# Performance work log

Hardware: AMD Instinct MI355X
Metric: run time of the kernel (lower is better)

Reference implementation:

```python
import jax, jax.numpy as jnp
import numpy as np
from jax.scipy.linalg import solve_triangular, cho_solve

K_SPARSE = 5
COMMIT = 0.25
EPS = 1e-10


def batch_omp(X, D, K):
    """Batched Orthogonal Matching Pursuit.
    X: [C, M] signals (columns). D: [C, N] L2-normalized dictionary.
    Returns support [M, K] (int32) and coefficients [M, K] in selection order.
    """
    G = D.T @ D                    # [N, N] Gram matrix
    h_bar = (D.T @ X).T            # [M, N] correlations
    M, N = h_bar.shape
    h = h_bar
    mask = jnp.ones((M, N), dtype=bool)
    gamma = jnp.zeros_like(h_bar)
    L = jnp.ones((M, 1, 1), dtype=X.dtype)
    rows = jnp.arange(M)
    I = None
    for k in range(1, K + 1):  # K is small and static -> unrolled
        idx = jnp.argmax(jnp.abs(h) * mask, axis=1)          # [M]
        mask = mask.at[rows, idx].set(False)
        if k > 1:
            G_col = G[I, idx[:, None]]                        # [M, k-1]
            w = solve_triangular(L, G_col[..., None], lower=True)[..., 0]  # [M, k-1]
            corner = jnp.sqrt(jnp.clip(1.0 - jnp.sum(w * w, axis=1), 1e-12))  # [M]
            top = jnp.concatenate([L, jnp.zeros((M, k - 1, 1), X.dtype)], axis=2)
            bot = jnp.concatenate([w[:, None, :], corner[:, None, None]], axis=2)
            L = jnp.concatenate([top, bot], axis=1)           # [M, k, k]
            I = jnp.concatenate([I, idx[:, None]], axis=1)
        else:
            I = idx[:, None]
        h_sel = h_bar[rows[:, None], I]                       # [M, k]
        gamma_sel = cho_solve((L, True), h_sel[..., None])[..., 0]  # [M, k]
        gamma = gamma.at[rows[:, None], I].set(gamma_sel)
        # beta = gamma_sel @ G[I]  -> residual update over all atoms
        beta = jnp.einsum('mk,mkn->mn', gamma_sel, G[I])      # [M, N]
        h = h_bar - beta
    coeffs = gamma[rows[:, None], I]                          # [M, K]
    return I, coeffs


def setup_inputs() -> dict:
    key = jax.random.key(0)
    k1, k2 = jax.random.split(key)
    z_e = jax.random.normal(k1, (8, 64, 64, 64), dtype=jnp.float32)        # [B, C, H, W]
    dictionary = jax.random.normal(k2, (64, 512), dtype=jnp.float32)       # [C, N]
    return {"z_e": z_e, "dictionary": dictionary}


def reference(z_e, dictionary):
    B, C, H, W = z_e.shape
    # [B,C,H,W] -> [C, B*H*W] column signals
    signals = z_e.transpose(0, 2, 3, 1).reshape(-1, C).T
    # L2-normalize dictionary columns (F.normalize with dim=0)
    norms = jnp.linalg.norm(dictionary, axis=0, keepdims=True)
    Dn = dictionary / jnp.maximum(norms, EPS)
    # OMP runs under no_grad in the original
    support, coeffs = batch_omp(jax.lax.stop_gradient(signals),
                                jax.lax.stop_gradient(Dn), K_SPARSE)
    # reconstruct: sum_k coeff_k * atom_k (gradient flows through Dn)
    atoms = Dn.T[support]                                     # [M, K, C]
    recon = jnp.einsum('mkc,mk->mc', atoms, coeffs)           # [M, C]
    z_dl = recon.reshape(B, H, W, C).transpose(0, 3, 1, 2)    # [B, C, H, W]
    dl_latent_loss = jnp.mean((z_dl - jax.lax.stop_gradient(z_e)) ** 2)
    e_latent_loss = jnp.mean((jax.lax.stop_gradient(z_dl) - z_e) ** 2)
    loss = dl_latent_loss + COMMIT * e_latent_loss
    z_dl_ste = z_e + jax.lax.stop_gradient(z_dl - z_e)        # straight-through
    return (z_dl_ste, loss,
            support.reshape(B, H, W, K_SPARSE),
            coeffs.reshape(B, H, W, K_SPARSE))
```

## Files before the change

### kernel.cpp

```cpp
#include <hip/hip_runtime.h>

#define NC 64
#define NA 512
#define KS 5

#define WS_DN   0
#define WS_DNT  32768
#define WS_G    65536
#define WS_ACCF 327680

#define OUT_LOSS 2097152
#define OUT_SUP  2097153
#define OUT_COF  2260993

__global__ void norm_kernel(const float* __restrict__ D, float* __restrict__ Dn,
                            float* __restrict__ DnT) {
  int n = blockIdx.x * 64 + threadIdx.x;
  float s = 0.f;
  for (int c = 0; c < NC; ++c) {
    float v = D[c * NA + n];
    s += v * v;
  }
  float den = fmaxf(sqrtf(s), 1e-10f);
  for (int c = 0; c < NC; ++c) {
    float v = D[c * NA + n] / den;
    Dn[c * NA + n]  = v;
    DnT[n * NC + c] = v;
  }
}

__global__ void gram_kernel(const float* __restrict__ Dn,
                            float* __restrict__ G, double* __restrict__ accum) {
  __shared__ float col[NC];
  int i = blockIdx.x, t = threadIdx.x;
  if (t < NC) col[t] = Dn[t * NA + i];
  if (i == 0 && t == 0) *accum = 0.0;
  __syncthreads();
  float s = 0.f;
#pragma unroll
  for (int c = 0; c < NC; ++c) s += col[c] * Dn[c * NA + t];
  G[(size_t)i * NA + t] = s;
}

template<int KK>
__device__ __forceinline__ void omp_stepH(
    const int hl, const float* __restrict__ G,
    const float* __restrict__ parkS,
    float (&h16)[16], unsigned &msk, int (&I)[KS],
    float (&Lo)[10], float (&rd)[KS], float (&gam)[KS]) {
  float bv = -1.f; int bn = 0;
#pragma unroll
  for (int s = 0; s < 16; ++s) {
    int a = ((s >> 2) << 7) + 4 * hl + (s & 3);
    float v = ((msk >> s) & 1u) ? fabsf(h16[s]) : 0.f;
    if (v > bv) { bv = v; bn = a; }
  }
#pragma unroll
  for (int off = 1; off < 32; off <<= 1) {
    float ov = __shfl_xor(bv, off);
    int   on = __shfl_xor(bn, off);
    if (ov > bv || (ov == bv && on < bn)) { bv = ov; bn = on; }
  }
  const int idx = bn;
  if (((idx & 127) >> 2) == hl)
    msk &= ~(1u << (((idx >> 7) << 2) | (idx & 3)));
  I[KK] = idx;

  if constexpr (KK == 0) {
    rd[0] = 1.f;
  } else {
    float Gc[KK], w_[KK];
#pragma unroll
    for (int j = 0; j < KK; ++j) Gc[j] = G[(size_t)I[j] * NA + idx];
#pragma unroll
    for (int i = 0; i < KK; ++i) {
      float ssum = Gc[i];
#pragma unroll
      for (int j = 0; j < i; ++j) ssum -= Lo[i*(i-1)/2 + j] * w_[j];
      w_[i] = ssum * rd[i];
    }
    float ww = 0.f;
#pragma unroll
    for (int i = 0; i < KK; ++i) ww += w_[i] * w_[i];
    float corner = sqrtf(fmaxf(1.f - ww, 1e-12f));
#pragma unroll
    for (int j = 0; j < KK; ++j) Lo[KK*(KK-1)/2 + j] = w_[j];
    rd[KK] = 1.f / corner;
  }

#pragma unroll
  for (int i = 0; i <= KK; ++i) {
    float b_ = parkS[I[i]];
#pragma unroll
    for (int j = 0; j < i; ++j) b_ -= Lo[i*(i-1)/2 + j] * gam[j];
    gam[i] = b_ * rd[i];
  }
#pragma unroll
  for (int i = KK; i >= 0; --i) {
    float g_ = gam[i];
#pragma unroll
    for (int j = i + 1; j <= KK; ++j) g_ -= Lo[j*(j-1)/2 + i] * gam[j];
    gam[i] = g_ * rd[i];
  }

  if constexpr (KK < 4) {
    const float4* pk4 = (const float4*)parkS;
#pragma unroll
    for (int i = 0; i < 4; ++i) {
      float4 hv = pk4[(i << 5) + hl];
      h16[i*4+0] = hv.x; h16[i*4+1] = hv.y; h16[i*4+2] = hv.z; h16[i*4+3] = hv.w;
    }
#pragma unroll
    for (int j = 0; j <= KK; ++j) {
      const float4* g4 = (const float4*)(G + (size_t)I[j] * NA);
      const float gj = gam[j];
#pragma unroll
      for (int i = 0; i < 4; ++i) {
        float4 g = g4[(i << 5) + hl];
        h16[i*4+0] -= gj * g.x; h16[i*4+1] -= gj * g.y;
        h16[i*4+2] -= gj * g.z; h16[i*4+3] -= gj * g.w;
      }
    }
  }
}

__global__ __launch_bounds__(256, 4) void omp_kernel(
    const float* __restrict__ z, const float* __restrict__ Dn,
    const float* __restrict__ DnT, const float* __restrict__ G,
    float* __restrict__ out, double* __restrict__ accum) {
  __shared__ __align__(16) float park[8 * NA];
  __shared__ float xsz[8 * NC];
  __shared__ double wsq[8];
  const int t = threadIdx.x, lane = t & 63, wv = t >> 6;
  const int hl = lane & 31;
  const int m0 = blockIdx.x * 8;
  const int bh = m0 >> 6, b = bh >> 6, h = bh & 63, w0 = m0 & 63;
  const size_t zbase = (size_t)b * 262144 + (size_t)h * 64 + w0;

  for (int j = t; j < 8 * NC; j += 256) {
    int c = j >> 3, s = j & 7;
    xsz[s * NC + c] = z[zbase + (size_t)c * 4096 + s];
  }
  __syncthreads();
  const int sig = wv * 2 + (lane >> 5);
  const float2 xf2 = *(const float2*)&xsz[sig * NC + 2 * hl];

  {
    float acc[8][2];
#pragma unroll
    for (int s = 0; s < 8; ++s) { acc[s][0] = 0.f; acc[s][1] = 0.f; }

    const float2* Dn2 = (const float2*)Dn + (wv << 6) + lane;
    const float4* zp4 = (const float4*)(z + zbase);
#pragma unroll 8
    for (int c = 0; c < 64; ++c) {
      float2 dv = Dn2[c << 8];
      float4 xa = zp4[(c << 10)];
      float4 xb = zp4[(c << 10) + 1];
      acc[0][0] += xa.x * dv.x; acc[0][1] += xa.x * dv.y;
      acc[1][0] += xa.y * dv.x; acc[1][1] += xa.y * dv.y;
      acc[2][0] += xa.z * dv.x; acc[2][1] += xa.z * dv.y;
      acc[3][0] += xa.w * dv.x; acc[3][1] += xa.w * dv.y;
      acc[4][0] += xb.x * dv.x; acc[4][1] += xb.x * dv.y;
      acc[5][0] += xb.y * dv.x; acc[5][1] += xb.y * dv.y;
      acc[6][0] += xb.z * dv.x; acc[6][1] += xb.z * dv.y;
      acc[7][0] += xb.w * dv.x; acc[7][1] += xb.w * dv.y;
    }
    float2* park2 = (float2*)park;
#pragma unroll
    for (int s = 0; s < 8; ++s)
      park2[(s << 8) + (wv << 6) + lane] = make_float2(acc[s][0], acc[s][1]);
  }
  __syncthreads();

  const float* parkS = park + (size_t)sig * NA;
  float h16[16];
  {
    const float4* pk4 = (const float4*)parkS;
#pragma unroll
    for (int i = 0; i < 4; ++i) {
      float4 hv = pk4[(i << 5) + hl];
      h16[i*4+0] = hv.x; h16[i*4+1] = hv.y; h16[i*4+2] = hv.z; h16[i*4+3] = hv.w;
    }
  }
  unsigned msk = 0xFFFFu;
  int I[KS];
  float Lo[10], rd[KS], gam[KS];

  omp_stepH<0>(hl, G, parkS, h16, msk, I, Lo, rd, gam);
  omp_stepH<1>(hl, G, parkS, h16, msk, I, Lo, rd, gam);
  omp_stepH<2>(hl, G, parkS, h16, msk, I, Lo, rd, gam);
  omp_stepH<3>(hl, G, parkS, h16, msk, I, Lo, rd, gam);
  omp_stepH<4>(hl, G, parkS, h16, msk, I, Lo, rd, gam);

  float rrA = 0.f, rrB = 0.f;
#pragma unroll
  for (int j = 0; j < KS; ++j) {
    const float2 dvv = ((const float2*)(DnT + (size_t)I[j] * NC))[hl];
    rrA += gam[j] * dvv.x;
    rrB += gam[j] * dvv.y;
  }
  const float dA = rrA - xf2.x, dB = rrB - xf2.y;
  xsz[(2 * hl) * 8 + sig]     = xf2.x + dA;
  xsz[(2 * hl + 1) * 8 + sig] = xf2.y + dB;
  double sq = (double)dA * (double)dA + (double)dB * (double)dB;
#pragma unroll
  for (int off = 1; off < 32; off <<= 1) sq += __shfl_xor(sq, off);
  if (hl == 0) wsq[sig] = sq;

  if (hl < KS) {
    int   iv = I[0];
    float gv = gam[0];
    if (hl == 1) { iv = I[1]; gv = gam[1]; }
    if (hl == 2) { iv = I[2]; gv = gam[2]; }
    if (hl == 3) { iv = I[3]; gv = gam[3]; }
    if (hl == 4) { iv = I[4]; gv = gam[4]; }
    const int m = m0 + sig;
    out[OUT_SUP + (size_t)m * KS + hl] = (float)iv;
    out[OUT_COF + (size_t)m * KS + hl] = gv;
  }

  __syncthreads();
  for (int j = t; j < 8 * NC; j += 256) {
    int c = j >> 3, s = j & 7;
    out[zbase + (size_t)c * 4096 + s] = xsz[j];
  }
  if (t == 0) {
    double ssum = 0.0;
#pragma unroll
    for (int i = 0; i < 8; ++i) ssum += wsq[i];
    atomicAdd(accum, ssum);
  }
}

__global__ void final_kernel(const double* __restrict__ accum, float* __restrict__ out) {
  double mse = *accum / 2097152.0;
  out[OUT_LOSS] = (float)(mse + 0.25 * mse);
}

extern "C" void kernel_launch(void* const* d_in, const int* in_sizes, int n_in,
                              void* d_out, int out_size, void* d_ws, size_t ws_size,
                              hipStream_t stream) {
  const float* z_e = (const float*)d_in[0];
  const float* dic = (const float*)d_in[1];
  float* out = (float*)d_out;
  float* ws = (float*)d_ws;
  float* Dn   = ws + WS_DN;
  float* DnT  = ws + WS_DNT;
  float* G    = ws + WS_G;
  double* accu = (double*)(ws + WS_ACCF);

  hipLaunchKernelGGL(norm_kernel,  dim3(8),    dim3(64),  0, stream, dic, Dn, DnT);
  hipLaunchKernelGGL(gram_kernel,  dim3(NA),   dim3(NA),  0, stream, Dn, G, accu);
  hipLaunchKernelGGL(omp_kernel,   dim3(4096), dim3(256), 0, stream,
                     z_e, Dn, DnT, G, out, accu);
  hipLaunchKernelGGL(final_kernel, dim3(1),    dim3(1),   0, stream, accu, out);
}
```

Baseline: 146.5 us.

## Process sixteen signals per block with 16-lane groups and incremental forward solve

Each OMP block now handles 16 signals instead of 8. Each signal is served by a 16-lane quarter-wave holding 32 correlation values per lane, replacing the 32-lane half-wave with 16 values. The correlation GEMM phase reuses each dictionary load across twice as many signals. The Cholesky forward substitution becomes incremental, computing only the new y entry per step instead of re-solving the whole system. The cost is higher register pressure (occupancy hint lowered from 4 to 2 blocks), double the shared memory per block, and half as many blocks.

Result: no change. 143.9 us (-1.8%).

```diff
diff --git a/kernel.cpp b/kernel.cpp
--- a/kernel.cpp
+++ b/kernel.cpp
@@ -43,31 +43,33 @@
 }
 
 template<int KK>
-__device__ __forceinline__ void omp_stepH(
-    const int hl, const float* __restrict__ G,
+__device__ __forceinline__ void omp_stepQ(
+    const int ql, const float* __restrict__ G,
     const float* __restrict__ parkS,
-    float (&h16)[16], unsigned &msk, int (&I)[KS],
-    float (&Lo)[10], float (&rd)[KS], float (&gam)[KS]) {
+    float (&h32)[32], unsigned &msk, int (&I)[KS],
+    float (&Lo)[10], float (&rd)[KS], float (&y)[KS], float (&gam)[KS]) {
   float bv = -1.f; int bn = 0;
 #pragma unroll
-  for (int s = 0; s < 16; ++s) {
-    int a = ((s >> 2) << 7) + 4 * hl + (s & 3);
-    float v = ((msk >> s) & 1u) ? fabsf(h16[s]) : 0.f;
+  for (int s = 0; s < 32; ++s) {
+    int a = ((s >> 2) << 6) + 4 * ql + (s & 3);
+    float v = ((msk >> s) & 1u) ? fabsf(h32[s]) : 0.f;
     if (v > bv) { bv = v; bn = a; }
   }
 #pragma unroll
-  for (int off = 1; off < 32; off <<= 1) {
+  for (int off = 1; off < 16; off <<= 1) {
     float ov = __shfl_xor(bv, off);
     int   on = __shfl_xor(bn, off);
     if (ov > bv || (ov == bv && on < bn)) { bv = ov; bn = on; }
   }
   const int idx = bn;
-  if (((idx & 127) >> 2) == hl)
-    msk &= ~(1u << (((idx >> 7) << 2) | (idx & 3)));
+  if (((idx & 63) >> 2) == ql)
+    msk &= ~(1u << (((idx >> 6) << 2) | (idx & 3)));
   I[KK] = idx;
+  const float bk = parkS[idx];
 
   if constexpr (KK == 0) {
     rd[0] = 1.f;
+    y[0] = bk * rd[0];
   } else {
     float Gc[KK], w_[KK];
 #pragma unroll
@@ -86,18 +88,15 @@
 #pragma unroll
     for (int j = 0; j < KK; ++j) Lo[KK*(KK-1)/2 + j] = w_[j];
     rd[KK] = 1.f / corner;
-  }
-
-#pragma unroll
-  for (int i = 0; i <= KK; ++i) {
-    float b_ = parkS[I[i]];
-#pragma unroll
-    for (int j = 0; j < i; ++j) b_ -= Lo[i*(i-1)/2 + j] * gam[j];
-    gam[i] = b_ * rd[i];
-  }
+    float fs = bk;
+#pragma unroll
+    for (int j = 0; j < KK; ++j) fs -= w_[j] * y[j];
+    y[KK] = fs * rd[KK];
+  }
+
 #pragma unroll
   for (int i = KK; i >= 0; --i) {
-    float g_ = gam[i];
+    float g_ = y[i];
 #pragma unroll
     for (int j = i + 1; j <= KK; ++j) g_ -= Lo[j*(j-1)/2 + i] * gam[j];
     gam[i] = g_ * rd[i];
@@ -106,129 +105,143 @@
   if constexpr (KK < 4) {
     const float4* pk4 = (const float4*)parkS;
 #pragma unroll
-    for (int i = 0; i < 4; ++i) {
-      float4 hv = pk4[(i << 5) + hl];
-      h16[i*4+0] = hv.x; h16[i*4+1] = hv.y; h16[i*4+2] = hv.z; h16[i*4+3] = hv.w;
+    for (int i = 0; i < 8; ++i) {
+      float4 hv = pk4[(i << 4) + ql];
+      h32[i*4+0] = hv.x; h32[i*4+1] = hv.y; h32[i*4+2] = hv.z; h32[i*4+3] = hv.w;
     }
 #pragma unroll
     for (int j = 0; j <= KK; ++j) {
       const float4* g4 = (const float4*)(G + (size_t)I[j] * NA);
       const float gj = gam[j];
 #pragma unroll
-      for (int i = 0; i < 4; ++i) {
-        float4 g = g4[(i << 5) + hl];
-        h16[i*4+0] -= gj * g.x; h16[i*4+1] -= gj * g.y;
-        h16[i*4+2] -= gj * g.z; h16[i*4+3] -= gj * g.w;
+      for (int i = 0; i < 8; ++i) {
+        float4 g = g4[(i << 4) + ql];
+        h32[i*4+0] -= gj * g.x; h32[i*4+1] -= gj * g.y;
+        h32[i*4+2] -= gj * g.z; h32[i*4+3] -= gj * g.w;
       }
     }
   }
 }
 
-__global__ __launch_bounds__(256, 4) void omp_kernel(
+__global__ __launch_bounds__(256, 2) void omp_kernel(
     const float* __restrict__ z, const float* __restrict__ Dn,
     const float* __restrict__ DnT, const float* __restrict__ G,
     float* __restrict__ out, double* __restrict__ accum) {
-  __shared__ __align__(16) float park[8 * NA];
-  __shared__ float xsz[8 * NC];
-  __shared__ double wsq[8];
+  __shared__ __align__(16) float park[16 * NA];
+  __shared__ __align__(16) float xsz[16 * NC];
+  __shared__ double wsq[16];
   const int t = threadIdx.x, lane = t & 63, wv = t >> 6;
-  const int hl = lane & 31;
-  const int m0 = blockIdx.x * 8;
+  const int ql = lane & 15;
+  const int m0 = blockIdx.x * 16;
   const int bh = m0 >> 6, b = bh >> 6, h = bh & 63, w0 = m0 & 63;
   const size_t zbase = (size_t)b * 262144 + (size_t)h * 64 + w0;
 
-  for (int j = t; j < 8 * NC; j += 256) {
-    int c = j >> 3, s = j & 7;
+  for (int j = t; j < 16 * NC; j += 256) {
+    int c = j >> 4, s = j & 15;
     xsz[s * NC + c] = z[zbase + (size_t)c * 4096 + s];
   }
   __syncthreads();
-  const int sig = wv * 2 + (lane >> 5);
-  const float2 xf2 = *(const float2*)&xsz[sig * NC + 2 * hl];
+  const int sig = (wv << 2) + (lane >> 4);
+  const float4 xf4 = *(const float4*)&xsz[sig * NC + 4 * ql];
 
   {
-    float acc[8][2];
-#pragma unroll
-    for (int s = 0; s < 8; ++s) { acc[s][0] = 0.f; acc[s][1] = 0.f; }
+    float acc[16][2];
+#pragma unroll
+    for (int s = 0; s < 16; ++s) { acc[s][0] = 0.f; acc[s][1] = 0.f; }
 
     const float2* Dn2 = (const float2*)Dn + (wv << 6) + lane;
     const float4* zp4 = (const float4*)(z + zbase);
-#pragma unroll 8
+#pragma unroll 4
     for (int c = 0; c < 64; ++c) {
       float2 dv = Dn2[c << 8];
-      float4 xa = zp4[(c << 10)];
+      float4 xa = zp4[(c << 10) + 0];
       float4 xb = zp4[(c << 10) + 1];
-      acc[0][0] += xa.x * dv.x; acc[0][1] += xa.x * dv.y;
-      acc[1][0] += xa.y * dv.x; acc[1][1] += xa.y * dv.y;
-      acc[2][0] += xa.z * dv.x; acc[2][1] += xa.z * dv.y;
-      acc[3][0] += xa.w * dv.x; acc[3][1] += xa.w * dv.y;
-      acc[4][0] += xb.x * dv.x; acc[4][1] += xb.x * dv.y;
-      acc[5][0] += xb.y * dv.x; acc[5][1] += xb.y * dv.y;
-      acc[6][0] += xb.z * dv.x; acc[6][1] += xb.z * dv.y;
-      acc[7][0] += xb.w * dv.x; acc[7][1] += xb.w * dv.y;
+      float4 xc = zp4[(c << 10) + 2];
+      float4 xd = zp4[(c << 10) + 3];
+      acc[ 0][0] += xa.x * dv.x; acc[ 0][1] += xa.x * dv.y;
+      acc[ 1][0] += xa.y * dv.x; acc[ 1][1] += xa.y * dv.y;
+      acc[ 2][0] += xa.z * dv.x; acc[ 2][1] += xa.z * dv.y;
+      acc[ 3][0] += xa.w * dv.x; acc[ 3][1] += xa.w * dv.y;
+      acc[ 4][0] += xb.x * dv.x; acc[ 4][1] += xb.x * dv.y;
+      acc[ 5][0] += xb.y * dv.x; acc[ 5][1] += xb.y * dv.y;
+      acc[ 6][0] += xb.z * dv.x; acc[ 6][1] += xb.z * dv.y;
+      acc[ 7][0] += xb.w * dv.x; acc[ 7][1] += xb.w * dv.y;
+      acc[ 8][0] += xc.x * dv.x; acc[ 8][1] += xc.x * dv.y;
+      acc[ 9][0] += xc.y * dv.x; acc[ 9][1] += xc.y * dv.y;
+      acc[10][0] += xc.z * dv.x; acc[10][1] += xc.z * dv.y;
+      acc[11][0] += xc.w * dv.x; acc[11][1] += xc.w * dv.y;
+      acc[12][0] += xd.x * dv.x; acc[12][1] += xd.x * dv.y;
+      acc[13][0] += xd.y * dv.x; acc[13][1] += xd.y * dv.y;
+      acc[14][0] += xd.z * dv.x; acc[14][1] += xd.z * dv.y;
+      acc[15][0] += xd.w * dv.x; acc[15][1] += xd.w * dv.y;
     }
     float2* park2 = (float2*)park;
 #pragma unroll
-    for (int s = 0; s < 8; ++s)
+    for (int s = 0; s < 16; ++s)
       park2[(s << 8) + (wv << 6) + lane] = make_float2(acc[s][0], acc[s][1]);
   }
   __syncthreads();
 
   const float* parkS = park + (size_t)sig * NA;
-  float h16[16];
+  float h32[32];
   {
     const float4* pk4 = (const float4*)parkS;
 #pragma unroll
-    for (int i = 0; i < 4; ++i) {
-      float4 hv = pk4[(i << 5) + hl];
-      h16[i*4+0] = hv.x; h16[i*4+1] = hv.y; h16[i*4+2] = hv.z; h16[i*4+3] = hv.w;
-    }
-  }
-  unsigned msk = 0xFFFFu;
+    for (int i = 0; i < 8; ++i) {
+      float4 hv = pk4[(i << 4) + ql];
+      h32[i*4+0] = hv.x; h32[i*4+1] = hv.y; h32[i*4+2] = hv.z; h32[i*4+3] = hv.w;
+    }
+  }
+  unsigned msk = 0xFFFFFFFFu;
   int I[KS];
-  float Lo[10], rd[KS], gam[KS];
-
-  omp_stepH<0>(hl, G, parkS, h16, msk, I, Lo, rd, gam);
-  omp_stepH<1>(hl, G, parkS, h16, msk, I, Lo, rd, gam);
-  omp_stepH<2>(hl, G, parkS, h16, msk, I, Lo, rd, gam);
-  omp_stepH<3>(hl, G, parkS, h16, msk, I, Lo, rd, gam);
-  omp_stepH<4>(hl, G, parkS, h16, msk, I, Lo, rd, gam);
-
-  float rrA = 0.f, rrB = 0.f;
+  float Lo[10], rd[KS], y[KS], gam[KS];
+
+  omp_stepQ<0>(ql, G, parkS, h32, msk, I, Lo, rd, y, gam);
+  omp_stepQ<1>(ql, G, parkS, h32, msk, I, Lo, rd, y, gam);
+  omp_stepQ<2>(ql, G, parkS, h32, msk, I, Lo, rd, y, gam);
+  omp_stepQ<3>(ql, G, parkS, h32, msk, I, Lo, rd, y, gam);
+  omp_stepQ<4>(ql, G, parkS, h32, msk, I, Lo, rd, y, gam);
+
+  float rr0 = 0.f, rr1 = 0.f, rr2 = 0.f, rr3 = 0.f;
 #pragma unroll
   for (int j = 0; j < KS; ++j) {
-    const float2 dvv = ((const float2*)(DnT + (size_t)I[j] * NC))[hl];
-    rrA += gam[j] * dvv.x;
-    rrB += gam[j] * dvv.y;
-  }
-  const float dA = rrA - xf2.x, dB = rrB - xf2.y;
-  xsz[(2 * hl) * 8 + sig]     = xf2.x + dA;
-  xsz[(2 * hl + 1) * 8 + sig] = xf2.y + dB;
-  double sq = (double)dA * (double)dA + (double)dB * (double)dB;
-#pragma unroll
-  for (int off = 1; off < 32; off <<= 1) sq += __shfl_xor(sq, off);
-  if (hl == 0) wsq[sig] = sq;
-
-  if (hl < KS) {
+    const float4 dvv = ((const float4*)(DnT + (size_t)I[j] * NC))[ql];
+    rr0 += gam[j] * dvv.x; rr1 += gam[j] * dvv.y;
+    rr2 += gam[j] * dvv.z; rr3 += gam[j] * dvv.w;
+  }
+  const float d0 = rr0 - xf4.x, d1 = rr1 - xf4.y;
+  const float d2 = rr2 - xf4.z, d3 = rr3 - xf4.w;
+  xsz[(4 * ql + 0) * 16 + sig] = xf4.x + d0;
+  xsz[(4 * ql + 1) * 16 + sig] = xf4.y + d1;
+  xsz[(4 * ql + 2) * 16 + sig] = xf4.z + d2;
+  xsz[(4 * ql + 3) * 16 + sig] = xf4.w + d3;
+  double sq = (double)d0 * (double)d0 + (double)d1 * (double)d1
+            + (double)d2 * (double)d2 + (double)d3 * (double)d3;
+#pragma unroll
+  for (int off = 1; off < 16; off <<= 1) sq += __shfl_xor(sq, off);
+  if (ql == 0) wsq[sig] = sq;
+
+  if (ql < KS) {
     int   iv = I[0];
     float gv = gam[0];
-    if (hl == 1) { iv = I[1]; gv = gam[1]; }
-    if (hl == 2) { iv = I[2]; gv = gam[2]; }
-    if (hl == 3) { iv = I[3]; gv = gam[3]; }
-    if (hl == 4) { iv = I[4]; gv = gam[4]; }
+    if (ql == 1) { iv = I[1]; gv = gam[1]; }
+    if (ql == 2) { iv = I[2]; gv = gam[2]; }
+    if (ql == 3) { iv = I[3]; gv = gam[3]; }
+    if (ql == 4) { iv = I[4]; gv = gam[4]; }
     const int m = m0 + sig;
-    out[OUT_SUP + (size_t)m * KS + hl] = (float)iv;
-    out[OUT_COF + (size_t)m * KS + hl] = gv;
-  }
-
-  __syncthreads();
-  for (int j = t; j < 8 * NC; j += 256) {
-    int c = j >> 3, s = j & 7;
+    out[OUT_SUP + (size_t)m * KS + ql] = (float)iv;
+    out[OUT_COF + (size_t)m * KS + ql] = gv;
+  }
+
+  __syncthreads();
+  for (int j = t; j < 16 * NC; j += 256) {
+    int c = j >> 4, s = j & 15;
     out[zbase + (size_t)c * 4096 + s] = xsz[j];
   }
   if (t == 0) {
     double ssum = 0.0;
 #pragma unroll
-    for (int i = 0; i < 8; ++i) ssum += wsq[i];
+    for (int i = 0; i < 16; ++i) ssum += wsq[i];
     atomicAdd(accum, ssum);
   }
 }
@@ -252,7 +265,7 @@
 
   hipLaunchKernelGGL(norm_kernel,  dim3(8),    dim3(64),  0, stream, dic, Dn, DnT);
   hipLaunchKernelGGL(gram_kernel,  dim3(NA),   dim3(NA),  0, stream, Dn, G, accu);
-  hipLaunchKernelGGL(omp_kernel,   dim3(4096), dim3(256), 0, stream,
+  hipLaunchKernelGGL(omp_kernel,   dim3(2048), dim3(256), 0, stream,
                      z_e, Dn, DnT, G, out, accu);
   hipLaunchKernelGGL(final_kernel, dim3(1),    dim3(1),   0, stream, accu, out);
 }
```
